# Kernel optimization log

Measured on AMD Instinct MI355X. Metric: run time of the kernel, lower is better.

The kernel has to match this reference:

```python
import jax, jax.numpy as jnp
import numpy as np

B, T = 128, 100
NOISE_STD = 0.1  # deterministic=False path

def leaky(x, slope):
    return jnp.where(x >= 0, x, slope * x)

def setup_inputs() -> dict:
    key = jax.random.key(0)
    ks = jax.random.split(key, 24)
    s = 0.02
    d = {}
    d["input_data"] = jax.random.normal(ks[0], (B, T, 3, 3), jnp.float32)
    d["eps"] = jax.random.normal(ks[1], (B, 64), jnp.float32)
    d["noise_eps"] = jax.random.normal(ks[2], (T, B, 4), jnp.float32)
    d["proj_W"] = jax.random.normal(ks[3], (4096, 9), jnp.float32) * s
    d["proj_b"] = jnp.zeros((4096,), jnp.float32)
    d["lstm_Wih"] = jax.random.normal(ks[4], (512, 4096), jnp.float32) * s
    d["lstm_Whh"] = jax.random.normal(ks[5], (512, 128), jnp.float32) * s
    d["lstm_bih"] = jnp.zeros((512,), jnp.float32)
    d["lstm_bhh"] = jnp.zeros((512,), jnp.float32)
    d["mu_W"] = jax.random.normal(ks[6], (64, 128), jnp.float32) * s
    d["mu_b"] = jnp.zeros((64,), jnp.float32)
    d["lv_W"] = jax.random.normal(ks[7], (64, 128), jnp.float32) * s
    d["lv_b"] = jnp.zeros((64,), jnp.float32)
    d["fcin_W"] = jax.random.normal(ks[8], (256, 64), jnp.float32) * s
    d["fcin_b"] = jnp.zeros((256,), jnp.float32)
    d["gru_Wih"] = jax.random.normal(ks[9], (783, 261), jnp.float32) * s
    d["gru_Whh"] = jax.random.normal(ks[10], (783, 261), jnp.float32) * s
    d["gru_bih"] = jnp.zeros((783,), jnp.float32)
    d["gru_bhh"] = jnp.zeros((783,), jnp.float32)
    d["jf_W1"] = jax.random.normal(ks[11], (64, 261), jnp.float32) * s
    d["jf_b1"] = jnp.zeros((64,), jnp.float32)
    d["jf_W2"] = jax.random.normal(ks[12], (9, 64), jnp.float32) * s
    d["jf_b2"] = jnp.zeros((9,), jnp.float32)
    return d

def reference(input_data, eps, noise_eps, proj_W, proj_b, lstm_Wih, lstm_Whh,
              lstm_bih, lstm_bhh, mu_W, mu_b, lv_W, lv_b, fcin_W, fcin_b,
              gru_Wih, gru_Whh, gru_bih, gru_bhh, jf_W1, jf_b1, jf_W2, jf_b2):
    b, t = input_data.shape[0], input_data.shape[1]
    pose = input_data.reshape(b, t, 9)
    # pose_projection: Linear(9, 4096) + LeakyReLU(0.1)
    proj = leaky(jnp.einsum('btj,kj->btk', pose, proj_W) + proj_b, 0.1)  # (B,T,4096)

    # LSTM over time, take final hidden state. PyTorch gate order: i,f,g,o.
    # Precompute input projections for all steps.
    x_gates = jnp.einsum('btk,gk->tbg', proj, lstm_Wih) + lstm_bih + lstm_bhh  # (T,B,512)
    hdim = 128
    def lstm_step(carry, xg):
        h, c = carry
        g = xg + h @ lstm_Whh.T  # (B,512)
        i, f, gg, o = jnp.split(g, 4, axis=-1)
        i, f, o = jax.nn.sigmoid(i), jax.nn.sigmoid(f), jax.nn.sigmoid(o)
        c = f * c + i * jnp.tanh(gg)
        h = o * jnp.tanh(c)
        return (h, c), None
    h0 = jnp.zeros((b, hdim), proj.dtype)
    (h_T, _), _ = jax.lax.scan(lstm_step, (h0, h0), x_gates)

    # VAE head (dropout in eval mode = identity)
    mu = leaky(h_T @ mu_W.T + mu_b, 0.1)
    logvar = jnp.clip(leaky(h_T @ lv_W.T + lv_b, 0.1), -10.0, 10.0)
    std = jnp.exp(0.5 * logvar)
    embedding = mu + eps * std

    x = embedding @ fcin_W.T + fcin_b  # (B,256)

    # Decoder GRU loop. PyTorch gate order: r,z,n; h' = (1-z)*n + z*h.
    noise = noise_eps * NOISE_STD  # (T,B,4)
    time_steps = (jnp.arange(t, dtype=x.dtype) / (t - 1))[:, None, None] * jnp.ones((t, b, 1), x.dtype)
    inp_seq = jnp.concatenate([jnp.broadcast_to(x[None], (t, b, 256)), noise, time_steps], axis=-1)  # (T,B,261)
    gx_seq = jnp.einsum('tbk,gk->tbg', inp_seq, gru_Wih) + gru_bih  # (T,B,783)

    def gru_step(h, gx):
        gh = h @ gru_Whh.T + gru_bhh
        gx_r, gx_z, gx_n = jnp.split(gx, 3, axis=-1)
        gh_r, gh_z, gh_n = jnp.split(gh, 3, axis=-1)
        r = jax.nn.sigmoid(gx_r + gh_r)
        z = jax.nn.sigmoid(gx_z + gh_z)
        n = jnp.tanh(gx_n + r * gh_n)
        h = (1.0 - z) * n + z * h
        frame = jax.nn.sigmoid(leaky(h @ jf_W1.T + jf_b1, 0.2) @ jf_W2.T + jf_b2)
        return h, frame

    h0g = jnp.zeros((b, 261), x.dtype)
    _, frames = jax.lax.scan(gru_step, h0g, gx_seq)  # (T,B,9)
    outputs = frames.transpose(1, 0, 2).reshape(b, t, 3, 3)
    return outputs, mu, logvar
```

## Files before the change

kernel.cpp:

```cpp
#include <hip/hip_runtime.h>
#include <hip/hip_bf16.h>

typedef float f32x4 __attribute__((ext_vector_type(4)));
typedef short s16x8 __attribute__((ext_vector_type(8)));

__device__ __forceinline__ float pv_sigm(float x){ return 1.0f/(1.0f + __expf(-x)); }
__device__ __forceinline__ float pv_tanh(float x){ float e = __expf(2.0f*x); return 1.0f - 2.0f/(e + 1.0f); }

__device__ __forceinline__ unsigned short pv_f2b(float x){
  union { float f; unsigned u; } c; c.f = x;
  unsigned r = (c.u + 0x7fffu + ((c.u >> 16) & 1u)) >> 16;
  return (unsigned short)r;
}
__device__ __forceinline__ unsigned pv_pack2(float a, float b){
  return ((unsigned)pv_f2b(b) << 16) | (unsigned)pv_f2b(a);
}
__device__ __forceinline__ float pv_lo(unsigned u){
  union { unsigned u; float f; } c; c.u = u << 16; return c.f;
}
__device__ __forceinline__ float pv_hi(unsigned u){
  union { unsigned u; float f; } c; c.u = u & 0xffff0000u; return c.f;
}

__device__ __forceinline__ unsigned char pv_fp8(float x){
  union { float f; unsigned u; } c; c.f = x;
  unsigned s = (c.u >> 24) & 0x80u;
  unsigned au = c.u & 0x7fffffffu;
  if (au == 0u) return (unsigned char)s;
  int ex = (int)(au >> 23) - 127;
  if (ex < -6) ex = -6;
  union { unsigned u; float f; } iv; iv.u = (unsigned)(3 - ex + 127) << 23;
  union { unsigned u; float f; } a;  a.u = au;
  int q = (int)rintf(a.f * iv.f);
  if (q >= 16) { q >>= 1; ex += 1; }
  unsigned bits;
  if (ex == -6 && q < 8) bits = (unsigned)q;
  else bits = (unsigned)(((ex + 7) << 3) | (q - 8));
  return (unsigned char)(s | bits);
}

#if defined(__has_builtin)
#if __has_builtin(__builtin_amdgcn_cvt_pk_fp8_f32)
#define PV_HW_FP8 1
#endif
#endif
__device__ __forceinline__ unsigned char pv_fp8_fast(float x){
#ifdef PV_HW_FP8
  return (unsigned char)__builtin_amdgcn_cvt_pk_fp8_f32(x, x, 0, false);
#else
  return pv_fp8(x);
#endif
}

__global__ void pv_prep_gru8(const float* Whh, const float* Wih,
                             unsigned long long* wfp8){
  int idx = blockIdx.x*256 + threadIdx.x;
  if (idx >= 29376) return;
  int T = idx / 576;
  int rem = idx - T*576;
  int c = rem >> 6;
  int l = rem & 63;
  int l16 = l & 15;
  int quad = l >> 4;
  int jb = T / 3;
  int ty = T - jb*3;
  int j = jb*16 + l16;
  int g = ty*261 + j;
  unsigned long long v = 0ull;
  #pragma unroll
  for (int e = 0; e < 8; ++e) {
    int k = c*32 + quad*8 + e;
    float w = 0.0f;
    if (j < 261) {
      if (k < 261) w = Whh[g*261 + k];
      else if (k < 266 && ty < 2) w = Wih[g*261 + 256 + (k - 261)];
    }
    v |= (unsigned long long)pv_fp8(8.0f*w) << (8*e);
  }
  wfp8[idx] = v;
}

__global__ __launch_bounds__(256) void pv_prep_wih(
    const float* __restrict__ Wih, unsigned* __restrict__ wihb)
{
  const int idx = blockIdx.x*256 + threadIdx.x;
  if (idx >= 262144) return;
  const float* src = Wih + idx*8;
  float4 a = *(const float4*)(src);
  float4 b = *(const float4*)(src + 4);
  uint4 o;
  o.x = pv_pack2(a.x, a.y);
  o.y = pv_pack2(a.z, a.w);
  o.z = pv_pack2(b.x, b.y);
  o.w = pv_pack2(b.z, b.w);
  *(uint4*)(wihb + idx*4) = o;
}

__global__ __launch_bounds__(512, 1) void pv_gemm3(
    const float* __restrict__ pose, const float* __restrict__ projW,
    const float* __restrict__ projb, const unsigned* __restrict__ wihb,
    const float* __restrict__ bih, const float* __restrict__ bhh,
    float* __restrict__ xg)
{
  __shared__ __align__(16) unsigned As2[128*20];
  __shared__ __align__(16) unsigned Bs2[2][512*20];
  __shared__ __align__(16) float Ws2[2][320];

  const int tid = threadIdx.x;
  const int m0 = blockIdx.x * 128;
  const int wave = tid >> 6, lane = tid & 63;
  const int wm = wave >> 2, wn = wave & 3;
  const int l16 = lane & 15, quad = lane >> 4;
  const int rl = tid >> 2, kq = tid & 3;

  float p[9];
  {
    const float* pr = pose + (m0 + rl)*9;
    #pragma unroll
    for (int j = 0; j < 9; ++j) p[j] = pr[j];
  }

  if (tid < 320) {
    Ws2[0][tid < 288 ? ((tid >> 5)*32 + (tid & 31)) : tid] =
        (tid < 288) ? projW[(tid & 31)*9 + (tid >> 5)] : projb[tid - 288];
  }
  #pragma unroll
  for (int i = 0; i < 4; ++i) {
    const int n = i*128 + rl;
    *(uint4*)(&Bs2[0][n*20 + kq*4]) = *(const uint4*)(wihb + n*2048 + kq*4);
  }
  __syncthreads();

  f32x4 acc[4][8];
  #pragma unroll
  for (int i = 0; i < 4; ++i)
    #pragma unroll
    for (int j = 0; j < 8; ++j) acc[i][j] = (f32x4){0.f,0.f,0.f,0.f};

  for (int kk = 0; kk < 128; ++kk) {
    const int cur = kk & 1, nxt = cur ^ 1;
    const int kn = kk + 1;

    uint4 bn0, bn1, bn2, bn3; float wv = 0.0f;
    if (kn < 128) {
      const unsigned* bsrc = wihb + kn*16 + kq*4;
      bn0 = *(const uint4*)(bsrc + (0*128 + rl)*2048);
      bn1 = *(const uint4*)(bsrc + (1*128 + rl)*2048);
      bn2 = *(const uint4*)(bsrc + (2*128 + rl)*2048);
      bn3 = *(const uint4*)(bsrc + (3*128 + rl)*2048);
      if (tid < 320)
        wv = (tid < 288) ? projW[kn*288 + (tid & 31)*9 + (tid >> 5)]
                         : projb[kn*32 + (tid - 288)];
    }

    {
      const float* W = Ws2[cur];
      f32x4 slo = *(const f32x4*)(W + 288 + kq*8);
      f32x4 shi = *(const f32x4*)(W + 292 + kq*8);
      #pragma unroll
      for (int j = 0; j < 9; ++j) {
        f32x4 wlo = *(const f32x4*)(W + j*32 + kq*8);
        f32x4 whi = *(const f32x4*)(W + j*32 + kq*8 + 4);
        slo += p[j]*wlo;
        shi += p[j]*whi;
      }
      #pragma unroll
      for (int e = 0; e < 4; ++e) {
        slo[e] = fmaxf(slo[e], 0.1f*slo[e]);
        shi[e] = fmaxf(shi[e], 0.1f*shi[e]);
      }
      uint4 av;
      av.x = pv_pack2(slo[0], slo[1]);
      av.y = pv_pack2(slo[2], slo[3]);
      av.z = pv_pack2(shi[0], shi[1]);
      av.w = pv_pack2(shi[2], shi[3]);
      *(uint4*)(&As2[rl*20 + kq*4]) = av;
    }

    if (kn < 128) {
      unsigned* bdst = &Bs2[nxt][rl*20 + kq*4];
      *(uint4*)(bdst + 0*128*20) = bn0;
      *(uint4*)(bdst + 1*128*20) = bn1;
      *(uint4*)(bdst + 2*128*20) = bn2;
      *(uint4*)(bdst + 3*128*20) = bn3;
      if (tid < 320)
        Ws2[nxt][tid < 288 ? ((tid >> 5)*32 + (tid & 31)) : tid] = wv;
    }
    __syncthreads();

    const unsigned short* As16 = (const unsigned short*)As2;
    const unsigned short* Bs16 = (const unsigned short*)Bs2[cur];
    s16x8 af[4];
    #pragma unroll
    for (int i = 0; i < 4; ++i)
      af[i] = *(const s16x8*)(As16 + (wm*64 + i*16 + l16)*40 + quad*8);
    #pragma unroll
    for (int j = 0; j < 8; ++j) {
      s16x8 bv = *(const s16x8*)(Bs16 + (wn*128 + j*16 + l16)*40 + quad*8);
      #pragma unroll
      for (int i = 0; i < 4; ++i)
        acc[i][j] = __builtin_amdgcn_mfma_f32_16x16x32_bf16(af[i], bv, acc[i][j], 0, 0, 0);
    }
    __syncthreads();
  }

  #pragma unroll
  for (int j = 0; j < 8; ++j) {
    int col = wn*128 + j*16 + l16;
    float bsum = bih[col] + bhh[col];
    #pragma unroll
    for (int i = 0; i < 4; ++i) {
      #pragma unroll
      for (int r = 0; r < 4; ++r) {
        int row = m0 + wm*64 + i*16 + quad*4 + r;
        int bb = row / 100;
        int tt = row - bb*100;
        xg[(tt*128 + bb)*512 + col] = acc[i][j][r] + bsum;
      }
    }
  }
}

__global__ __launch_bounds__(256) void pv_gemm(
    const float* pose, const float* projW, const float* projb,
    const float* Wih, const float* bih, const float* bhh,
    float* xg)
{
  __shared__ __align__(16) unsigned As[128*24];
  __shared__ __align__(16) unsigned Bs[128*24];
  __shared__ float Ws[320];

  const int tid = threadIdx.x;
  const int m0 = blockIdx.x * 128;
  const int n0 = blockIdx.y * 128;

  const int rl = tid >> 1;
  const int kh = tid & 1;
  float p0,p1,p2,p3,p4,p5,p6,p7,p8;
  {
    const float* pr = pose + (m0 + rl) * 9;
    p0=pr[0]; p1=pr[1]; p2=pr[2]; p3=pr[3]; p4=pr[4];
    p5=pr[5]; p6=pr[6]; p7=pr[7]; p8=pr[8];
  }

  const int wave = tid >> 6;
  const int lane = tid & 63;
  const int wm = wave >> 1, wn = wave & 1;
  const int l16 = lane & 15, quad = lane >> 4;

  f32x4 acc[4][4];
  #pragma unroll
  for (int i = 0; i < 4; ++i)
    #pragma unroll
    for (int j = 0; j < 4; ++j) acc[i][j] = (f32x4){0.f,0.f,0.f,0.f};

  for (int kk = 0; kk < 128; ++kk) {
    __syncthreads();
    for (int idx = tid; idx < 320; idx += 256)
      Ws[idx] = (idx < 288) ? projW[kk*288 + idx] : projb[kk*32 + (idx - 288)];
    #pragma unroll
    for (int i = 0; i < 8; ++i) {
      int q = tid + i*256;
      int nl = q >> 4;
      int kp = q & 15;
      const float* src = Wih + (n0 + nl)*4096 + kk*32 + kp*2;
      Bs[nl*24 + kp] = pv_pack2(src[0], src[1]);
    }
    __syncthreads();
    {
      const int kbase = kh*16;
      const float* wbase = Ws + kbase*9;
      float av[16];
      #pragma unroll
      for (int u = 0; u < 16; ++u) {
        const float* wr = wbase + u*9;
        float s = Ws[288 + kbase + u]
                + p0*wr[0] + p1*wr[1] + p2*wr[2] + p3*wr[3] + p4*wr[4]
                + p5*wr[5] + p6*wr[6] + p7*wr[7] + p8*wr[8];
        av[u] = fmaxf(s, 0.1f*s);
      }
      #pragma unroll
      for (int q = 0; q < 8; ++q)
        As[rl*24 + kh*8 + q] = pv_pack2(av[2*q], av[2*q+1]);
    }
    __syncthreads();
    const unsigned short* As16 = (const unsigned short*)As;
    const unsigned short* Bs16 = (const unsigned short*)Bs;
    s16x8 af[4], bfv[4];
    #pragma unroll
    for (int i = 0; i < 4; ++i)
      af[i] = *(const s16x8*)(As16 + (wm*64 + i*16 + l16)*48 + quad*8);
    #pragma unroll
    for (int j = 0; j < 4; ++j)
      bfv[j] = *(const s16x8*)(Bs16 + (wn*64 + j*16 + l16)*48 + quad*8);
    #pragma unroll
    for (int i = 0; i < 4; ++i)
      #pragma unroll
      for (int j = 0; j < 4; ++j)
        acc[i][j] = __builtin_amdgcn_mfma_f32_16x16x32_bf16(af[i], bfv[j], acc[i][j], 0, 0, 0);
  }
  #pragma unroll
  for (int j = 0; j < 4; ++j) {
    int col = n0 + wn*64 + j*16 + l16;
    float bsum = bih[col] + bhh[col];
    #pragma unroll
    for (int i = 0; i < 4; ++i) {
      #pragma unroll
      for (int r = 0; r < 4; ++r) {
        int row = m0 + wm*64 + i*16 + quad*4 + r;
        int bb = row / 100;
        int tt = row - bb*100;
        xg[(tt*128 + bb)*512 + col] = acc[i][j][r] + bsum;
      }
    }
  }
}

__global__ __launch_bounds__(512, 1) void pv_lstm2(
    const float* __restrict__ xg, const float* __restrict__ Whh,
    float* __restrict__ hT)
{
  __shared__ __align__(16) unsigned short Hs2[2][16*136];
  const int tid = threadIdx.x;
  const int wv = tid >> 6;
  const int lane = tid & 63;
  const int l16 = lane & 15, quad = lane >> 4;
  const int m0 = blockIdx.x * 16;
  const int j = wv*16 + l16;

  s16x8 bfr[4][4];
  #pragma unroll
  for (int ty = 0; ty < 4; ++ty) {
    const int g = ty*128 + j;
    #pragma unroll
    for (int c = 0; c < 4; ++c) {
      s16x8 v;
      #pragma unroll
      for (int e = 0; e < 8; ++e)
        v[e] = (short)pv_f2b(Whh[g*128 + c*32 + quad*8 + e]);
      bfr[ty][c] = v;
    }
  }
  for (int i = tid; i < 2*16*136; i += 512) ((unsigned short*)Hs2)[i] = 0;

  float cst[4] = {0.f, 0.f, 0.f, 0.f};
  const float* xbase = xg + (m0 + quad*4)*512 + j;

  float xv[4][4];
  #pragma unroll
  for (int r = 0; r < 4; ++r)
    #pragma unroll
    for (int ty = 0; ty < 4; ++ty)
      xv[r][ty] = xbase[(0*128 + r)*512 + ty*128];
  __syncthreads();

  for (int t = 0; t < 100; ++t) {
    const int cur = t & 1, nxt = cur ^ 1;
    float xn[4][4];
    if (t < 99) {
      #pragma unroll
      for (int r = 0; r < 4; ++r)
        #pragma unroll
        for (int ty = 0; ty < 4; ++ty)
          xn[r][ty] = xbase[((t+1)*128 + r)*512 + ty*128];
    }
    f32x4 acc[4];
    #pragma unroll
    for (int ty = 0; ty < 4; ++ty) acc[ty] = (f32x4){0.f,0.f,0.f,0.f};
    #pragma unroll
    for (int c = 0; c < 4; ++c) {
      s16x8 a = *(const s16x8*)(&Hs2[cur][l16*136 + c*32 + quad*8]);
      #pragma unroll
      for (int ty = 0; ty < 4; ++ty)
        acc[ty] = __builtin_amdgcn_mfma_f32_16x16x32_bf16(a, bfr[ty][c], acc[ty], 0, 0, 0);
    }
    #pragma unroll
    for (int r = 0; r < 4; ++r) {
      float gi = acc[0][r] + xv[r][0];
      float gf = acc[1][r] + xv[r][1];
      float gg = acc[2][r] + xv[r][2];
      float go = acc[3][r] + xv[r][3];
      float c_ = pv_sigm(gf)*cst[r] + pv_sigm(gi)*pv_tanh(gg);
      cst[r] = c_;
      float h = pv_sigm(go)*pv_tanh(c_);
      Hs2[nxt][(quad*4 + r)*136 + j] = pv_f2b(h);
      if (t == 99) hT[(m0 + quad*4 + r)*128 + j] = h;
    }
    if (t < 99) {
      #pragma unroll
      for (int r = 0; r < 4; ++r)
        #pragma unroll
        for (int ty = 0; ty < 4; ++ty)
          xv[r][ty] = xn[r][ty];
    }
    __syncthreads();
  }
}

__global__ __launch_bounds__(64) void pv_head(
    const float* hT, const float* eps,
    const float* muW, const float* mub,
    const float* lvW, const float* lvb,
    const float* fcW, const float* fcb,
    float* xvec, float* out)
{
  __shared__ float hrow[128];
  __shared__ float emb[64];
  const int b = blockIdx.x, j = threadIdx.x;
  hrow[j] = hT[b*128 + j];
  hrow[j + 64] = hT[b*128 + 64 + j];
  __syncthreads();
  float sm = mub[j], sl = lvb[j];
  for (int k = 0; k < 128; ++k) {
    sm += hrow[k]*muW[j*128 + k];
    sl += hrow[k]*lvW[j*128 + k];
  }
  float mu = fmaxf(sm, 0.1f*sm);
  float lv = fmaxf(sl, 0.1f*sl);
  lv = fminf(fmaxf(lv, -10.0f), 10.0f);
  float em = mu + eps[b*64 + j]*__expf(0.5f*lv);
  emb[j] = em;
  out[115200 + b*64 + j] = mu;
  out[123392 + b*64 + j] = lv;
  __syncthreads();
  for (int c4 = 0; c4 < 4; ++c4) {
    int c = c4*64 + j;
    float s = fcb[c];
    for (int k = 0; k < 64; ++k) s += emb[k]*fcW[c*64 + k];
    xvec[b*256 + c] = s;
  }
}

__global__ __launch_bounds__(256) void pv_gxbase(
    const float* xvec, const float* Wih,
    const float* bih, const float* bhh, float* gxb)
{
  __shared__ float xs[8*256];
  const int tid = threadIdx.x;
  const int bg = blockIdx.x;
  const int gg = blockIdx.y;
  for (int i = tid; i < 2048; i += 256) xs[i] = xvec[bg*2048 + i];
  __syncthreads();
  const int g = gg*256 + tid;
  if (g >= 783) return;
  float bias = bih[g] + ((g < 522) ? bhh[g] : 0.0f);
  float a0=bias,a1=bias,a2=bias,a3=bias,a4=bias,a5=bias,a6=bias,a7=bias;
  const float* wr = Wih + g*261;
  for (int k = 0; k < 256; ++k) {
    float w = wr[k];
    a0 += xs[0*256 + k]*w; a1 += xs[1*256 + k]*w;
    a2 += xs[2*256 + k]*w; a3 += xs[3*256 + k]*w;
    a4 += xs[4*256 + k]*w; a5 += xs[5*256 + k]*w;
    a6 += xs[6*256 + k]*w; a7 += xs[7*256 + k]*w;
  }
  gxb[(bg*8 + 0)*783 + g] = a0; gxb[(bg*8 + 1)*783 + g] = a1;
  gxb[(bg*8 + 2)*783 + g] = a2; gxb[(bg*8 + 3)*783 + g] = a3;
  gxb[(bg*8 + 4)*783 + g] = a4; gxb[(bg*8 + 5)*783 + g] = a5;
  gxb[(bg*8 + 6)*783 + g] = a6; gxb[(bg*8 + 7)*783 + g] = a7;
}

__global__ __launch_bounds__(512, 1) void pv_gru5(
    const float* __restrict__ gxb, const unsigned long long* __restrict__ wfp8,
    const float* __restrict__ Wih, const float* __restrict__ bhh,
    const float* __restrict__ noise, float* __restrict__ hseq)
{
  __shared__ __align__(16) unsigned long long Bl[27*9*64];
  __shared__ __align__(16) unsigned char A2[16*296];
  __shared__ __align__(16) float Ds[4*792];
  const int tid = threadIdx.x;
  const int wv = tid >> 6;
  const int lane = tid & 63;
  const int l16 = lane & 15, quad = lane >> 4;
  const int m0 = blockIdx.x * 4;
  const int tailOwner = (wv >= 5);

  long bfr[3][9];
  #pragma unroll
  for (int s = 0; s < 3; ++s)
    #pragma unroll
    for (int c = 0; c < 9; ++c)
      bfr[s][c] = (long)wfp8[((3*wv + s)*9 + c)*64 + lane];
  #pragma unroll
  for (int s = 0; s < 3; ++s)
    #pragma unroll
    for (int c = 0; c < 9; ++c)
      asm volatile("" : "+v"(bfr[s][c]));

  const int r_u = tid & 3;
  const int j1 = tid >> 2;
  const int j2 = 128 + j1;
  const int hasE3 = (tid < 20);
  const int j3 = 256 + (tid >> 2);
  float gx1[3], gx2[3], gx3[3], wn1[5], wn2[5], wn3[5];
  float bh1, bh2, bh3 = 0.f, h1 = 0.f, h2 = 0.f, h3 = 0.f;
  {
    const float* gb = gxb + (m0 + r_u)*783;
    gx1[0] = gb[j1]; gx1[1] = gb[261 + j1]; gx1[2] = gb[522 + j1];
    gx2[0] = gb[j2]; gx2[1] = gb[261 + j2]; gx2[2] = gb[522 + j2];
    const float* w1 = Wih + (522 + j1)*261 + 256;
    wn1[0] = 0.1f*w1[0]; wn1[1] = 0.1f*w1[1]; wn1[2] = 0.1f*w1[2];
    wn1[3] = 0.1f*w1[3]; wn1[4] = w1[4];
    const float* w2 = Wih + (522 + j2)*261 + 256;
    wn2[0] = 0.1f*w2[0]; wn2[1] = 0.1f*w2[1]; wn2[2] = 0.1f*w2[2];
    wn2[3] = 0.1f*w2[3]; wn2[4] = w2[4];
    bh1 = bhh[522 + j1];
    bh2 = bhh[522 + j2];
    #pragma unroll
    for (int k = 0; k < 3; ++k) gx3[k] = 0.f;
    #pragma unroll
    for (int k = 0; k < 5; ++k) wn3[k] = 0.f;
    if (hasE3) {
      gx3[0] = gb[j3]; gx3[1] = gb[261 + j3]; gx3[2] = gb[522 + j3];
      const float* w3 = Wih + (522 + j3)*261 + 256;
      wn3[0] = 0.1f*w3[0]; wn3[1] = 0.1f*w3[1]; wn3[2] = 0.1f*w3[2];
      wn3[3] = 0.1f*w3[3]; wn3[4] = w3[4];
      bh3 = bhh[522 + j3];
    }
  }

  for (int i = tid; i < 27*9*64; i += 512) Bl[i] = wfp8[24*9*64 + i];
  for (int i = tid; i < 4736; i += 512) A2[i] = 0;
  __syncthreads();
  if (tid < 20) {
    const int m = tid/5, i = tid - (tid/5)*5;
    float v = (i < 4) ? noise[(m0 + m)*4 + i]*0.1f : 0.0f;
    A2[m*296 + 261 + i] = pv_fp8(4.0f*v);
  }
  __syncthreads();

  const float inv32 = 1.0f/32.0f;
  const float* nptr = noise + (m0 + r_u)*4;
  for (int t = 0; t < 100; ++t) {
    const float4 ne = *(const float4*)(nptr + t*512);

    f32x4 acc[7];
    #pragma unroll
    for (int s = 0; s < 7; ++s) acc[s] = (f32x4){0,0,0,0};
    #pragma unroll
    for (int c = 0; c < 9; ++c) {
      const long a = *(const long*)(&A2[l16*296 + c*32 + quad*8]);
      acc[0] = __builtin_amdgcn_mfma_f32_16x16x32_fp8_fp8(a, bfr[0][c], acc[0], 0, 0, 0);
      acc[1] = __builtin_amdgcn_mfma_f32_16x16x32_fp8_fp8(a, bfr[1][c], acc[1], 0, 0, 0);
      acc[2] = __builtin_amdgcn_mfma_f32_16x16x32_fp8_fp8(a, bfr[2][c], acc[2], 0, 0, 0);
      const long b3 = (long)Bl[((3*wv + 0)*9 + c)*64 + lane];
      const long b4 = (long)Bl[((3*wv + 1)*9 + c)*64 + lane];
      const long b5 = (long)Bl[((3*wv + 2)*9 + c)*64 + lane];
      acc[3] = __builtin_amdgcn_mfma_f32_16x16x32_fp8_fp8(a, b3, acc[3], 0, 0, 0);
      acc[4] = __builtin_amdgcn_mfma_f32_16x16x32_fp8_fp8(a, b4, acc[4], 0, 0, 0);
      acc[5] = __builtin_amdgcn_mfma_f32_16x16x32_fp8_fp8(a, b5, acc[5], 0, 0, 0);
      if (tailOwner) {
        const long b6 = (long)Bl[((24 + (wv - 5))*9 + c)*64 + lane];
        acc[6] = __builtin_amdgcn_mfma_f32_16x16x32_fp8_fp8(a, b6, acc[6], 0, 0, 0);
      }
    }
    if (quad == 0) {
      #pragma unroll
      for (int s = 0; s < 3; ++s) {
        const int g = s*261 + wv*16 + l16;
        #pragma unroll
        for (int r = 0; r < 4; ++r) Ds[r*792 + g] = acc[s][r];
      }
      #pragma unroll
      for (int s = 0; s < 3; ++s) {
        const int g = s*261 + (8 + wv)*16 + l16;
        #pragma unroll
        for (int r = 0; r < 4; ++r) Ds[r*792 + g] = acc[3 + s][r];
      }
      if (tailOwner && l16 < 5) {
        const int g = (wv - 5)*261 + 256 + l16;
        #pragma unroll
        for (int r = 0; r < 4; ++r) Ds[r*792 + g] = acc[6][r];
      }
    }
    __syncthreads();

    {
      const float tv = (float)t * (1.0f/99.0f);
      const float* dsr = Ds + r_u*792;
      {
        float Dr = dsr[j1]*inv32 + gx1[0];
        float Dz = dsr[261 + j1]*inv32 + gx1[1];
        float Dn = dsr[522 + j1]*inv32;
        float nterm = ne.x*wn1[0] + ne.y*wn1[1] + ne.z*wn1[2]
                    + ne.w*wn1[3] + tv*wn1[4];
        float r_ = pv_sigm(Dr);
        float z_ = pv_sigm(Dz);
        float n_ = pv_tanh(gx1[2] + nterm + r_*(Dn + bh1));
        h1 = (1.0f - z_)*n_ + z_*h1;
        hseq[(t*128 + m0 + r_u)*261 + j1] = h1;
        A2[r_u*296 + j1] = pv_fp8_fast(4.0f*h1);
      }
      {
        float Dr = dsr[j2]*inv32 + gx2[0];
        float Dz = dsr[261 + j2]*inv32 + gx2[1];
        float Dn = dsr[522 + j2]*inv32;
        float nterm = ne.x*wn2[0] + ne.y*wn2[1] + ne.z*wn2[2]
                    + ne.w*wn2[3] + tv*wn2[4];
        float r_ = pv_sigm(Dr);
        float z_ = pv_sigm(Dz);
        float n_ = pv_tanh(gx2[2] + nterm + r_*(Dn + bh2));
        h2 = (1.0f - z_)*n_ + z_*h2;
        hseq[(t*128 + m0 + r_u)*261 + j2] = h2;
        A2[r_u*296 + j2] = pv_fp8_fast(4.0f*h2);
      }
      if (hasE3) {
        float Dr = dsr[j3]*inv32 + gx3[0];
        float Dz = dsr[261 + j3]*inv32 + gx3[1];
        float Dn = dsr[522 + j3]*inv32;
        float nterm = ne.x*wn3[0] + ne.y*wn3[1] + ne.z*wn3[2]
                    + ne.w*wn3[3] + tv*wn3[4];
        float r_ = pv_sigm(Dr);
        float z_ = pv_sigm(Dz);
        float n_ = pv_tanh(gx3[2] + nterm + r_*(Dn + bh3));
        h3 = (1.0f - z_)*n_ + z_*h3;
        hseq[(t*128 + m0 + r_u)*261 + j3] = h3;
        A2[r_u*296 + j3] = pv_fp8_fast(4.0f*h3);
      }
    }
    if (t < 99 && tid >= 40 && tid < 60) {
      const int k = tid - 40;
      const int m = k/5, i = k - (k/5)*5;
      float v = (i < 4) ? noise[((t+1)*128 + m0 + m)*4 + i]*0.1f
                        : (t+1)*(1.0f/99.0f);
      A2[m*296 + 261 + i] = pv_fp8(4.0f*v);
    }
    __syncthreads();
  }
}

__global__ __launch_bounds__(256) void pv_frames(
    const float* hseq, const float* W1, const float* b1,
    const float* W2, const float* b2, float* out)
{
  __shared__ __align__(16) float h16[16*264];
  __shared__ unsigned w1p[64*133];
  __shared__ float f1s[16*66];
  __shared__ float w2s[576];
  const int tid = threadIdx.x;
  const int r0 = blockIdx.x * 16;
  for (int i = tid; i < 16*264; i += 256) {
    int r = i / 264, k = i - r*264;
    h16[i] = (k < 261) ? hseq[(r0 + r)*261 + k] : 0.0f;
  }
  for (int i = tid; i < 64*131; i += 256) {
    int c = i/131, kp = i - (i/131)*131;
    int k = kp*2;
    float a0 = W1[c*261 + k];
    float a1 = (k + 1 < 261) ? W1[c*261 + k + 1] : 0.0f;
    w1p[c*133 + kp] = pv_pack2(a0, a1);
  }
  for (int i = tid; i < 576; i += 256) w2s[i] = W2[i];
  __syncthreads();
  #pragma unroll
  for (int e = 0; e < 4; ++e) {
    const int el = tid + e*256;
    const int r = el >> 6, c = el & 63;
    float s = b1[c];
    const unsigned* wp = w1p + c*133;
    const float* hr = h16 + r*264;
    for (int kp = 0; kp < 131; ++kp) {
      unsigned w = wp[kp];
      s += pv_lo(w)*hr[2*kp] + pv_hi(w)*hr[2*kp + 1];
    }
    f1s[r*66 + c] = fmaxf(s, 0.2f*s);
  }
  __syncthreads();
  if (tid < 144) {
    const int r = tid/9, oc = tid - (tid/9)*9;
    float s = b2[oc];
    const float* fr = f1s + r*66;
    const float* w = w2s + oc*64;
    #pragma unroll 8
    for (int k = 0; k < 64; ++k) s += fr[k]*w[k];
    const int rt = r0 + r;
    const int tt = rt >> 7, bb = rt & 127;
    out[bb*900 + tt*9 + oc] = pv_sigm(s);
  }
}

extern "C" __attribute__((visibility("default")))
void kernel_launch(void* const* d_in, const int* in_sizes, int n_in,
                   void* d_out, int out_size, void* d_ws, size_t ws_size,
                   hipStream_t stream)
{
  (void)in_sizes; (void)n_in; (void)out_size;
  const float* input_data = (const float*)d_in[0];
  const float* eps        = (const float*)d_in[1];
  const float* noise_eps  = (const float*)d_in[2];
  const float* proj_W     = (const float*)d_in[3];
  const float* proj_b     = (const float*)d_in[4];
  const float* lstm_Wih   = (const float*)d_in[5];
  const float* lstm_Whh   = (const float*)d_in[6];
  const float* lstm_bih   = (const float*)d_in[7];
  const float* lstm_bhh   = (const float*)d_in[8];
  const float* mu_W       = (const float*)d_in[9];
  const float* mu_b       = (const float*)d_in[10];
  const float* lv_W       = (const float*)d_in[11];
  const float* lv_b       = (const float*)d_in[12];
  const float* fcin_W     = (const float*)d_in[13];
  const float* fcin_b     = (const float*)d_in[14];
  const float* gru_Wih    = (const float*)d_in[15];
  const float* gru_Whh    = (const float*)d_in[16];
  const float* gru_bih    = (const float*)d_in[17];
  const float* gru_bhh    = (const float*)d_in[18];
  const float* jf_W1      = (const float*)d_in[19];
  const float* jf_b1      = (const float*)d_in[20];
  const float* jf_W2      = (const float*)d_in[21];
  const float* jf_b2      = (const float*)d_in[22];

  char* w = (char*)d_ws;
  float*              xg   = (float*)(w);
  unsigned long long* wfp8 = (unsigned long long*)(w + 26214400);
  float*              hT   = (float*)(w + 26449408);
  float*              xvec = (float*)(w + 26514944);
  float*              gxb  = (float*)(w + 26646016);
  float*              hseq = (float*)(w + 27046912);
  unsigned*           wihb = (unsigned*)(w + 40410112);
  float*              outf = (float*)d_out;

  const int use_split = (ws_size >= (size_t)44604416ull);

  pv_prep_gru8<<<115, 256, 0, stream>>>(gru_Whh, gru_Wih, wfp8);
  if (use_split) {
    pv_prep_wih<<<1024, 256, 0, stream>>>(lstm_Wih, wihb);
    pv_gemm3<<<100, 512, 0, stream>>>(input_data, proj_W, proj_b, wihb,
                                      lstm_bih, lstm_bhh, xg);
  } else {
    pv_gemm<<<dim3(100, 4), 256, 0, stream>>>(input_data, proj_W, proj_b,
                                              lstm_Wih, lstm_bih, lstm_bhh, xg);
  }
  pv_lstm2<<<8, 512, 0, stream>>>(xg, lstm_Whh, hT);
  pv_head<<<128, 64, 0, stream>>>(hT, eps, mu_W, mu_b, lv_W, lv_b,
                                  fcin_W, fcin_b, xvec, outf);
  pv_gxbase<<<dim3(16, 4), 256, 0, stream>>>(xvec, gru_Wih, gru_bih, gru_bhh, gxb);
  pv_gru5<<<32, 512, 0, stream>>>(gxb, wfp8, gru_Wih, gru_bhh, noise_eps, hseq);
  pv_frames<<<800, 256, 0, stream>>>(hseq, jf_W1, jf_b1, jf_W2, jf_b2, outf);
}
```

Baseline: 810.9 us.

## Rebalance GRU weight tiles into registers, pack LDS tiles, and defer stores

In the GRU recurrence kernel, each wave now holds four fp8 weight tiles in registers instead of three. The LDS tiles are repacked so two tiles load with one 16-byte read, and the last three tiles go into a separate small buffer. Hidden-state stores to global memory are moved to the start of the next step, and the next step's noise is prefetched, so neither sits on the critical path. In the input-projection GEMM, the MFMA block now runs before the stores that fill the next B buffer, with an extra barrier, so shared-memory writes overlap the math. The cost is more register pressure and an extra synchronisation per GEMM k-iteration.

```diff
diff --git a/kernel.cpp b/kernel.cpp
--- a/kernel.cpp
+++ b/kernel.cpp
@@ -3,6 +3,7 @@
 
 typedef float f32x4 __attribute__((ext_vector_type(4)));
 typedef short s16x8 __attribute__((ext_vector_type(8)));
+typedef long lgx2 __attribute__((ext_vector_type(2)));
 
 __device__ __forceinline__ float pv_sigm(float x){ return 1.0f/(1.0f + __expf(-x)); }
 __device__ __forceinline__ float pv_tanh(float x){ float e = __expf(2.0f*x); return 1.0f - 2.0f/(e + 1.0f); }
@@ -176,6 +177,23 @@
       av.w = pv_pack2(shi[2], shi[3]);
       *(uint4*)(&As2[rl*20 + kq*4]) = av;
     }
+    __syncthreads();
+
+    {
+      const unsigned short* As16 = (const unsigned short*)As2;
+      const unsigned short* Bs16 = (const unsigned short*)Bs2[cur];
+      s16x8 af[4];
+      #pragma unroll
+      for (int i = 0; i < 4; ++i)
+        af[i] = *(const s16x8*)(As16 + (wm*64 + i*16 + l16)*40 + quad*8);
+      #pragma unroll
+      for (int j = 0; j < 8; ++j) {
+        s16x8 bv = *(const s16x8*)(Bs16 + (wn*128 + j*16 + l16)*40 + quad*8);
+        #pragma unroll
+        for (int i = 0; i < 4; ++i)
+          acc[i][j] = __builtin_amdgcn_mfma_f32_16x16x32_bf16(af[i], bv, acc[i][j], 0, 0, 0);
+      }
+    }
 
     if (kn < 128) {
       unsigned* bdst = &Bs2[nxt][rl*20 + kq*4];
@@ -185,21 +203,6 @@
       *(uint4*)(bdst + 3*128*20) = bn3;
       if (tid < 320)
         Ws2[nxt][tid < 288 ? ((tid >> 5)*32 + (tid & 31)) : tid] = wv;
-    }
-    __syncthreads();
-
-    const unsigned short* As16 = (const unsigned short*)As2;
-    const unsigned short* Bs16 = (const unsigned short*)Bs2[cur];
-    s16x8 af[4];
-    #pragma unroll
-    for (int i = 0; i < 4; ++i)
-      af[i] = *(const s16x8*)(As16 + (wm*64 + i*16 + l16)*40 + quad*8);
-    #pragma unroll
-    for (int j = 0; j < 8; ++j) {
-      s16x8 bv = *(const s16x8*)(Bs16 + (wn*128 + j*16 + l16)*40 + quad*8);
-      #pragma unroll
-      for (int i = 0; i < 4; ++i)
-        acc[i][j] = __builtin_amdgcn_mfma_f32_16x16x32_bf16(af[i], bv, acc[i][j], 0, 0, 0);
     }
     __syncthreads();
   }
@@ -459,12 +462,13 @@
   gxb[(bg*8 + 6)*783 + g] = a6; gxb[(bg*8 + 7)*783 + g] = a7;
 }
 
-__global__ __launch_bounds__(512, 1) void pv_gru5(
+__global__ __launch_bounds__(512, 1) void pv_gru6(
     const float* __restrict__ gxb, const unsigned long long* __restrict__ wfp8,
     const float* __restrict__ Wih, const float* __restrict__ bhh,
     const float* __restrict__ noise, float* __restrict__ hseq)
 {
-  __shared__ __align__(16) unsigned long long Bl[27*9*64];
+  __shared__ __align__(16) unsigned long long Bp[9*8*128];
+  __shared__ __align__(16) unsigned long long Bt[9*3*64];
   __shared__ __align__(16) unsigned char A2[16*296];
   __shared__ __align__(16) float Ds[4*792];
   const int tid = threadIdx.x;
@@ -474,14 +478,14 @@
   const int m0 = blockIdx.x * 4;
   const int tailOwner = (wv >= 5);
 
-  long bfr[3][9];
-  #pragma unroll
-  for (int s = 0; s < 3; ++s)
+  long bfr[4][9];
+  #pragma unroll
+  for (int s = 0; s < 4; ++s)
     #pragma unroll
     for (int c = 0; c < 9; ++c)
-      bfr[s][c] = (long)wfp8[((3*wv + s)*9 + c)*64 + lane];
-  #pragma unroll
-  for (int s = 0; s < 3; ++s)
+      bfr[s][c] = (long)wfp8[((4*wv + s)*9 + c)*64 + lane];
+  #pragma unroll
+  for (int s = 0; s < 4; ++s)
     #pragma unroll
     for (int c = 0; c < 9; ++c)
       asm volatile("" : "+v"(bfr[s][c]));
@@ -518,7 +522,18 @@
     }
   }
 
-  for (int i = tid; i < 27*9*64; i += 512) Bl[i] = wfp8[24*9*64 + i];
+  for (int i = tid; i < 16*9*64; i += 512) {
+    const int T2 = i / 576;
+    const int rem = i - T2*576;
+    const int c = rem >> 6, ln = rem & 63;
+    Bp[(c*8 + (T2 >> 1))*128 + ln*2 + (T2 & 1)] = wfp8[((32 + T2)*9 + c)*64 + ln];
+  }
+  for (int i = tid; i < 3*9*64; i += 512) {
+    const int q = i / 576;
+    const int rem = i - q*576;
+    const int c = rem >> 6, ln = rem & 63;
+    Bt[(c*3 + q)*64 + ln] = wfp8[((48 + q)*9 + c)*64 + ln];
+  }
   for (int i = tid; i < 4736; i += 512) A2[i] = 0;
   __syncthreads();
   if (tid < 20) {
@@ -530,8 +545,16 @@
 
   const float inv32 = 1.0f/32.0f;
   const float* nptr = noise + (m0 + r_u)*4;
+  float4 ne = *(const float4*)(nptr);
   for (int t = 0; t < 100; ++t) {
-    const float4 ne = *(const float4*)(nptr + t*512);
+    if (t > 0) {
+      float* hrow = hseq + ((t-1)*128 + m0 + r_u)*261;
+      hrow[j1] = h1;
+      hrow[j2] = h2;
+      if (hasE3) hrow[j3] = h3;
+    }
+    float4 ne_n;
+    if (t < 99) ne_n = *(const float4*)(nptr + (t+1)*512);
 
     f32x4 acc[7];
     #pragma unroll
@@ -542,29 +565,29 @@
       acc[0] = __builtin_amdgcn_mfma_f32_16x16x32_fp8_fp8(a, bfr[0][c], acc[0], 0, 0, 0);
       acc[1] = __builtin_amdgcn_mfma_f32_16x16x32_fp8_fp8(a, bfr[1][c], acc[1], 0, 0, 0);
       acc[2] = __builtin_amdgcn_mfma_f32_16x16x32_fp8_fp8(a, bfr[2][c], acc[2], 0, 0, 0);
-      const long b3 = (long)Bl[((3*wv + 0)*9 + c)*64 + lane];
-      const long b4 = (long)Bl[((3*wv + 1)*9 + c)*64 + lane];
-      const long b5 = (long)Bl[((3*wv + 2)*9 + c)*64 + lane];
-      acc[3] = __builtin_amdgcn_mfma_f32_16x16x32_fp8_fp8(a, b3, acc[3], 0, 0, 0);
-      acc[4] = __builtin_amdgcn_mfma_f32_16x16x32_fp8_fp8(a, b4, acc[4], 0, 0, 0);
-      acc[5] = __builtin_amdgcn_mfma_f32_16x16x32_fp8_fp8(a, b5, acc[5], 0, 0, 0);
+      acc[3] = __builtin_amdgcn_mfma_f32_16x16x32_fp8_fp8(a, bfr[3][c], acc[3], 0, 0, 0);
+      const lgx2 bp = *(const lgx2*)(&Bp[(c*8 + wv)*128 + lane*2]);
+      acc[4] = __builtin_amdgcn_mfma_f32_16x16x32_fp8_fp8(a, bp[0], acc[4], 0, 0, 0);
+      acc[5] = __builtin_amdgcn_mfma_f32_16x16x32_fp8_fp8(a, bp[1], acc[5], 0, 0, 0);
       if (tailOwner) {
-        const long b6 = (long)Bl[((24 + (wv - 5))*9 + c)*64 + lane];
+        const long b6 = (long)Bt[(c*3 + (wv - 5))*64 + lane];
         acc[6] = __builtin_amdgcn_mfma_f32_16x16x32_fp8_fp8(a, b6, acc[6], 0, 0, 0);
       }
     }
     if (quad == 0) {
       #pragma unroll
-      for (int s = 0; s < 3; ++s) {
-        const int g = s*261 + wv*16 + l16;
+      for (int s = 0; s < 4; ++s) {
+        const int T = 4*wv + s;
+        const int g = (T % 3)*261 + (T / 3)*16 + l16;
         #pragma unroll
         for (int r = 0; r < 4; ++r) Ds[r*792 + g] = acc[s][r];
       }
       #pragma unroll
-      for (int s = 0; s < 3; ++s) {
-        const int g = s*261 + (8 + wv)*16 + l16;
+      for (int s = 0; s < 2; ++s) {
+        const int T = 32 + 2*wv + s;
+        const int g = (T % 3)*261 + (T / 3)*16 + l16;
         #pragma unroll
-        for (int r = 0; r < 4; ++r) Ds[r*792 + g] = acc[3 + s][r];
+        for (int r = 0; r < 4; ++r) Ds[r*792 + g] = acc[4 + s][r];
       }
       if (tailOwner && l16 < 5) {
         const int g = (wv - 5)*261 + 256 + l16;
@@ -587,7 +610,6 @@
         float z_ = pv_sigm(Dz);
         float n_ = pv_tanh(gx1[2] + nterm + r_*(Dn + bh1));
         h1 = (1.0f - z_)*n_ + z_*h1;
-        hseq[(t*128 + m0 + r_u)*261 + j1] = h1;
         A2[r_u*296 + j1] = pv_fp8_fast(4.0f*h1);
       }
       {
@@ -600,7 +622,6 @@
         float z_ = pv_sigm(Dz);
         float n_ = pv_tanh(gx2[2] + nterm + r_*(Dn + bh2));
         h2 = (1.0f - z_)*n_ + z_*h2;
-        hseq[(t*128 + m0 + r_u)*261 + j2] = h2;
         A2[r_u*296 + j2] = pv_fp8_fast(4.0f*h2);
       }
       if (hasE3) {
@@ -613,9 +634,9 @@
         float z_ = pv_sigm(Dz);
         float n_ = pv_tanh(gx3[2] + nterm + r_*(Dn + bh3));
         h3 = (1.0f - z_)*n_ + z_*h3;
-        hseq[(t*128 + m0 + r_u)*261 + j3] = h3;
         A2[r_u*296 + j3] = pv_fp8_fast(4.0f*h3);
       }
+      ne = (t < 99) ? ne_n : ne;
     }
     if (t < 99 && tid >= 40 && tid < 60) {
       const int k = tid - 40;
@@ -625,6 +646,12 @@
       A2[m*296 + 261 + i] = pv_fp8(4.0f*v);
     }
     __syncthreads();
+  }
+  {
+    float* hrow = hseq + (99*128 + m0 + r_u)*261;
+    hrow[j1] = h1;
+    hrow[j2] = h2;
+    if (hasE3) hrow[j3] = h3;
   }
 }
 
@@ -733,6 +760,6 @@
   pv_head<<<128, 64, 0, stream>>>(hT, eps, mu_W, mu_b, lv_W, lv_b,
                                   fcin_W, fcin_b, xvec, outf);
   pv_gxbase<<<dim3(16, 4), 256, 0, stream>>>(xvec, gru_Wih, gru_bih, gru_bhh, gxb);
-  pv_gru5<<<32, 512, 0, stream>>>(gxb, wfp8, gru_Wih, gru_bhh, noise_eps, hseq);
+  pv_gru6<<<32, 512, 0, stream>>>(gxb, wfp8, gru_Wih, gru_bhh, noise_eps, hseq);
   pv_frames<<<800, 256, 0, stream>>>(hseq, jf_W1, jf_b1, jf_W2, jf_b2, outf);
 }
```

Measured after the change: 843.7 us. +4.0%, slower.

## Split LSTM input GEMM across N into two column blocks per row tile

Applied to the files above, without the earlier changes.

The fused projection+LSTM-input GEMM now launches a 100x2 grid where each block computes 256 of the 512 gate columns instead of all 512. That gives 200 blocks rather than 100, so more of the GPU's CUs are busy, and it halves per-block B-tile shared memory and accumulators. The loop body is also reordered: the MFMA compute now runs right after the A tile is written and before the next B tile is stored. The cost is that each block recomputes the 9->4096 pose projection and leaky ReLU for its row tile, doubling that work overall.

```diff
diff --git a/kernel.cpp b/kernel.cpp
--- a/kernel.cpp
+++ b/kernel.cpp
@@ -96,22 +96,24 @@
   *(uint4*)(wihb + idx*4) = o;
 }
 
-__global__ __launch_bounds__(512, 1) void pv_gemm3(
+__global__ __launch_bounds__(512, 1) void pv_gemm4(
     const float* __restrict__ pose, const float* __restrict__ projW,
     const float* __restrict__ projb, const unsigned* __restrict__ wihb,
     const float* __restrict__ bih, const float* __restrict__ bhh,
     float* __restrict__ xg)
 {
   __shared__ __align__(16) unsigned As2[128*20];
-  __shared__ __align__(16) unsigned Bs2[2][512*20];
+  __shared__ __align__(16) unsigned Bs2[2][256*20];
   __shared__ __align__(16) float Ws2[2][320];
 
   const int tid = threadIdx.x;
   const int m0 = blockIdx.x * 128;
+  const int n0 = blockIdx.y * 256;
   const int wave = tid >> 6, lane = tid & 63;
   const int wm = wave >> 2, wn = wave & 3;
   const int l16 = lane & 15, quad = lane >> 4;
   const int rl = tid >> 2, kq = tid & 3;
+  const int rb = tid >> 1, hb = tid & 1;
 
   float p[9];
   {
@@ -124,30 +126,28 @@
     Ws2[0][tid < 288 ? ((tid >> 5)*32 + (tid & 31)) : tid] =
         (tid < 288) ? projW[(tid & 31)*9 + (tid >> 5)] : projb[tid - 288];
   }
-  #pragma unroll
-  for (int i = 0; i < 4; ++i) {
-    const int n = i*128 + rl;
-    *(uint4*)(&Bs2[0][n*20 + kq*4]) = *(const uint4*)(wihb + n*2048 + kq*4);
-  }
-  __syncthreads();
-
-  f32x4 acc[4][8];
+  {
+    const unsigned* src = wihb + (n0 + rb)*2048 + hb*8;
+    *(uint4*)(&Bs2[0][rb*20 + hb*8])     = *(const uint4*)(src);
+    *(uint4*)(&Bs2[0][rb*20 + hb*8 + 4]) = *(const uint4*)(src + 4);
+  }
+  __syncthreads();
+
+  f32x4 acc[4][4];
   #pragma unroll
   for (int i = 0; i < 4; ++i)
     #pragma unroll
-    for (int j = 0; j < 8; ++j) acc[i][j] = (f32x4){0.f,0.f,0.f,0.f};
+    for (int j = 0; j < 4; ++j) acc[i][j] = (f32x4){0.f,0.f,0.f,0.f};
 
   for (int kk = 0; kk < 128; ++kk) {
     const int cur = kk & 1, nxt = cur ^ 1;
     const int kn = kk + 1;
 
-    uint4 bn0, bn1, bn2, bn3; float wv = 0.0f;
+    uint4 bn0, bn1; float wv = 0.0f;
     if (kn < 128) {
-      const unsigned* bsrc = wihb + kn*16 + kq*4;
-      bn0 = *(const uint4*)(bsrc + (0*128 + rl)*2048);
-      bn1 = *(const uint4*)(bsrc + (1*128 + rl)*2048);
-      bn2 = *(const uint4*)(bsrc + (2*128 + rl)*2048);
-      bn3 = *(const uint4*)(bsrc + (3*128 + rl)*2048);
+      const unsigned* bsrc = wihb + (n0 + rb)*2048 + kn*16 + hb*8;
+      bn0 = *(const uint4*)(bsrc);
+      bn1 = *(const uint4*)(bsrc + 4);
       if (tid < 320)
         wv = (tid < 288) ? projW[kn*288 + (tid & 31)*9 + (tid >> 5)]
                          : projb[kn*32 + (tid - 288)];
@@ -176,37 +176,36 @@
       av.w = pv_pack2(shi[2], shi[3]);
       *(uint4*)(&As2[rl*20 + kq*4]) = av;
     }
+    __syncthreads();
+
+    {
+      const unsigned short* As16 = (const unsigned short*)As2;
+      const unsigned short* Bs16 = (const unsigned short*)Bs2[cur];
+      s16x8 af[4];
+      #pragma unroll
+      for (int i = 0; i < 4; ++i)
+        af[i] = *(const s16x8*)(As16 + (wm*64 + i*16 + l16)*40 + quad*8);
+      #pragma unroll
+      for (int j = 0; j < 4; ++j) {
+        s16x8 bv = *(const s16x8*)(Bs16 + (wn*64 + j*16 + l16)*40 + quad*8);
+        #pragma unroll
+        for (int i = 0; i < 4; ++i)
+          acc[i][j] = __builtin_amdgcn_mfma_f32_16x16x32_bf16(af[i], bv, acc[i][j], 0, 0, 0);
+      }
+    }
 
     if (kn < 128) {
-      unsigned* bdst = &Bs2[nxt][rl*20 + kq*4];
-      *(uint4*)(bdst + 0*128*20) = bn0;
-      *(uint4*)(bdst + 1*128*20) = bn1;
-      *(uint4*)(bdst + 2*128*20) = bn2;
-      *(uint4*)(bdst + 3*128*20) = bn3;
+      *(uint4*)(&Bs2[nxt][rb*20 + hb*8])     = bn0;
+      *(uint4*)(&Bs2[nxt][rb*20 + hb*8 + 4]) = bn1;
       if (tid < 320)
         Ws2[nxt][tid < 288 ? ((tid >> 5)*32 + (tid & 31)) : tid] = wv;
     }
     __syncthreads();
-
-    const unsigned short* As16 = (const unsigned short*)As2;
-    const unsigned short* Bs16 = (const unsigned short*)Bs2[cur];
-    s16x8 af[4];
-    #pragma unroll
-    for (int i = 0; i < 4; ++i)
-      af[i] = *(const s16x8*)(As16 + (wm*64 + i*16 + l16)*40 + quad*8);
-    #pragma unroll
-    for (int j = 0; j < 8; ++j) {
-      s16x8 bv = *(const s16x8*)(Bs16 + (wn*128 + j*16 + l16)*40 + quad*8);
-      #pragma unroll
-      for (int i = 0; i < 4; ++i)
-        acc[i][j] = __builtin_amdgcn_mfma_f32_16x16x32_bf16(af[i], bv, acc[i][j], 0, 0, 0);
-    }
-    __syncthreads();
-  }
-
-  #pragma unroll
-  for (int j = 0; j < 8; ++j) {
-    int col = wn*128 + j*16 + l16;
+  }
+
+  #pragma unroll
+  for (int j = 0; j < 4; ++j) {
+    int col = n0 + wn*64 + j*16 + l16;
     float bsum = bih[col] + bhh[col];
     #pragma unroll
     for (int i = 0; i < 4; ++i) {
@@ -723,8 +722,8 @@
   pv_prep_gru8<<<115, 256, 0, stream>>>(gru_Whh, gru_Wih, wfp8);
   if (use_split) {
     pv_prep_wih<<<1024, 256, 0, stream>>>(lstm_Wih, wihb);
-    pv_gemm3<<<100, 512, 0, stream>>>(input_data, proj_W, proj_b, wihb,
-                                      lstm_bih, lstm_bhh, xg);
+    pv_gemm4<<<dim3(100, 2), 512, 0, stream>>>(input_data, proj_W, proj_b, wihb,
+                                               lstm_bih, lstm_bhh, xg);
   } else {
     pv_gemm<<<dim3(100, 4), 256, 0, stream>>>(input_data, proj_W, proj_b,
                                               lstm_Wih, lstm_bih, lstm_bhh, xg);
```

Result: faster. 747.8 us (-7.8%).
